# Optimization experiments

Measured on AMD Instinct MI355X. Metric: run time of the kernel, lower is better.

## Reference

```python
import jax, jax.numpy as jnp
import numpy as np

B, S, D = 1024, 60, 256   # seq_len=60 is hard-coded by nn.Linear(dim*60, n_experts)
H = 1024                  # d_inner
E = 8                     # n_experts
TOPK = 2
CAP = B * TOPK // E       # balanced per-expert capacity = 256


def setup_inputs() -> dict:
    key = jax.random.key(0)
    ks = jax.random.split(key, 9)
    s = 0.02
    return {
        "x":        jax.random.normal(ks[0], (B, S, D), dtype=jnp.float32),
        "W_switch": jax.random.normal(ks[1], (S * D, E), dtype=jnp.float32) * s,
        "b_switch": jnp.zeros((E,), dtype=jnp.float32),
        "W1":       jax.random.normal(ks[2], (E, D, H), dtype=jnp.float32) * s,
        "b1":       jnp.zeros((E, H), dtype=jnp.float32),
        "W2":       jax.random.normal(ks[3], (E, H, D), dtype=jnp.float32) * s,
        "b2":       jnp.zeros((E, D), dtype=jnp.float32),
        "gamma":    jnp.ones((D,), dtype=jnp.float32),
        "beta":     jnp.zeros((D,), dtype=jnp.float32),
    }


def reference(x, W_switch, b_switch, W1, b1, W2, b2, gamma, beta):
    # --- routing: softmax over experts per batch element ---
    logits = x.reshape(B, S * D) @ W_switch + b_switch          # [B, E]
    probs = jax.nn.softmax(logits, axis=-1)
    # balanced dispatch: each expert takes its top-CAP batch indices
    _, idx = jax.lax.top_k(probs.T, CAP)                        # [E, CAP] int32
    xe = x[idx]                                                 # gather -> [E, CAP, S, D]
    # --- per-expert grouped GEMMs (Column- then Row-parallel linear) ---
    h = jax.nn.gelu(jnp.einsum('ecsd,edh->ecsh', xe, W1)
                    + b1[:, None, None, :], approximate=False)  # [E, CAP, S, H]
    oe = jnp.einsum('ecsh,ehd->ecsd', h, W2) + b2[:, None, None, :]  # [E, CAP, S, D]
    # --- scatter-combine via index_add over the batch dim ---
    out = jnp.zeros_like(x).at[idx.reshape(-1)].add(oe.reshape(E * CAP, S, D))
    # --- residual + post-LayerNorm (pre_lnorm=False) ---
    z = x + out
    mu = jnp.mean(z, axis=-1, keepdims=True)
    var = jnp.var(z, axis=-1, keepdims=True)
    return (z - mu) * jax.lax.rsqrt(var + 1e-5) * gamma + beta
```

## Files before the change

### kernel.cpp

```cpp
#include <hip/hip_runtime.h>
#include <hip/hip_bf16.h>
#include <math.h>

#define NB   1024
#define NS   60
#define ND   256
#define NH   1024
#define NE   8
#define NCAP 256
#define NTOK (NCAP*NS)
#define BM   64
#define NBLK (NTOK/BM)

typedef __attribute__((ext_vector_type(8)))  short short8;
typedef __attribute__((ext_vector_type(16))) float floatx16;

__device__ __forceinline__ unsigned short f2bf(float f) {
    union { float f; unsigned u; } cv; cv.f = f;
    unsigned u = cv.u;
    u += 0x7FFFu + ((u >> 16) & 1u);
    return (unsigned short)(u >> 16);
}
__device__ __forceinline__ float bf2f(unsigned short h) {
    union { unsigned u; float f; } c; c.u = ((unsigned)h) << 16; return c.f;
}
__device__ __forceinline__ unsigned pk2bf(float a, float b) {
    return (unsigned)f2bf(a) | ((unsigned)f2bf(b) << 16);
}

__global__ void k_pack(const float* __restrict__ W1, const float* __restrict__ W2,
                       unsigned short* __restrict__ W1t, unsigned short* __restrict__ W2t) {
    int idx = blockIdx.x * 256 + threadIdx.x;
    if (idx < 524288) {
        int h4 = idx & 255;
        int k  = (idx >> 8) & 255;
        int e  = idx >> 16;
        float4 w = *(const float4*)(W1 + ((size_t)(e * 256 + k)) * 1024 + h4 * 4);
        float wv[4] = {w.x, w.y, w.z, w.w};
        int lane_k = ((k >> 3) & 1) * 32;
        int kt = k >> 4, j = k & 7;
#pragma unroll
        for (int c = 0; c < 4; ++c) {
            int h = h4 * 4 + c;
            int frag = (e * 32 + (h >> 5)) * 16 + kt;
            W1t[(size_t)frag * 512 + ((h & 31) + lane_k) * 8 + j] = f2bf(wv[c]);
        }
    } else {
        int i2 = idx - 524288;
        int d4 = i2 & 63;
        int h  = (i2 >> 6) & 1023;
        int e  = i2 >> 16;
        float4 w = *(const float4*)(W2 + ((size_t)(e * 1024 + h)) * 256 + d4 * 4);
        float wv[4] = {w.x, w.y, w.z, w.w};
        int lane_k = ((h >> 3) & 1) * 32;
        int kt = h >> 4, j = h & 7;
#pragma unroll
        for (int c = 0; c < 4; ++c) {
            int d = d4 * 4 + c;
            int frag = (e * 8 + (d >> 5)) * 64 + kt;
            W2t[(size_t)frag * 512 + ((d & 31) + lane_k) * 8 + j] = f2bf(wv[c]);
        }
    }
}

__global__ __launch_bounds__(256)
void k_route(const float* __restrict__ x, const float* __restrict__ Wsw,
             unsigned short* __restrict__ xb, float* __restrict__ partials) {
    int g = blockIdx.x & 127;
    int s = blockIdx.x >> 7;
    int team = threadIdx.x >> 5;
    int j = threadIdx.x & 31;
    int b = g * 8 + team;
    const float* xr = x + (size_t)b * 15360 + s * 1920;
    unsigned short* xbr = xb + (size_t)b * 15360 + s * 1920;
    float a[8];
#pragma unroll
    for (int e = 0; e < 8; ++e) a[e] = 0.f;
    for (int it = 0; it < 15; ++it) {
        int k = it * 128 + j * 4;
        float4 xv = *(const float4*)(xr + k);
        ushort4 o;
        o.x = f2bf(xv.x); o.y = f2bf(xv.y); o.z = f2bf(xv.z); o.w = f2bf(xv.w);
        *(ushort4*)(xbr + k) = o;
        float xa[4] = {xv.x, xv.y, xv.z, xv.w};
        const float* w = Wsw + (size_t)(s * 1920 + k) * 8;
#pragma unroll
        for (int c = 0; c < 4; ++c) {
            float4 w0 = *(const float4*)(w + c * 8);
            float4 w1 = *(const float4*)(w + c * 8 + 4);
            float xc = xa[c];
            a[0] += xc * w0.x; a[1] += xc * w0.y; a[2] += xc * w0.z; a[3] += xc * w0.w;
            a[4] += xc * w1.x; a[5] += xc * w1.y; a[6] += xc * w1.z; a[7] += xc * w1.w;
        }
    }
#pragma unroll
    for (int m = 16; m >= 1; m >>= 1) {
#pragma unroll
        for (int e = 0; e < 8; ++e) a[e] += __shfl_xor(a[e], m);
    }
    if (j == 0) {
        float4* p = (float4*)(partials + ((size_t)(s * 1024) + b) * 8);
        p[0] = make_float4(a[0], a[1], a[2], a[3]);
        p[1] = make_float4(a[4], a[5], a[6], a[7]);
    }
}

__global__ __launch_bounds__(256)
void k_topk(const float* __restrict__ partials, const float* __restrict__ bsw,
            int* __restrict__ idxb, int* __restrict__ cntb, int* __restrict__ slotb) {
    __shared__ float v[NB];
    int e = blockIdx.x >> 2;
    int q = blockIdx.x & 3;
    int tid = threadIdx.x;
    float bs[8];
#pragma unroll
    for (int i = 0; i < 8; ++i) bs[i] = bsw[i];
#pragma unroll
    for (int rr = 0; rr < 4; ++rr) {
        int row = rr * 256 + tid;
        float l[8];
#pragma unroll
        for (int i = 0; i < 8; ++i) l[i] = bs[i];
#pragma unroll
        for (int s = 0; s < 8; ++s) {
            const float4* p = (const float4*)(partials + ((size_t)(s * 1024) + row) * 8);
            float4 p0 = p[0], p1 = p[1];
            l[0] += p0.x; l[1] += p0.y; l[2] += p0.z; l[3] += p0.w;
            l[4] += p1.x; l[5] += p1.y; l[6] += p1.z; l[7] += p1.w;
        }
        float m = l[0];
#pragma unroll
        for (int i = 1; i < 8; ++i) m = fmaxf(m, l[i]);
        float sum = 0.f;
#pragma unroll
        for (int i = 0; i < 8; ++i) sum += expf(l[i] - m);
        v[row] = expf(l[e] - m) / sum;
    }
    __syncthreads();
    int cand = q * 256 + tid;
    float mv = v[cand];
    int cnt = 0;
    for (int jj = 0; jj < NB; ++jj) {
        float vj = v[jj];
        cnt += (vj > mv) || (vj == mv && jj < cand);
    }
    if (cnt < NCAP) {
        idxb[e * NCAP + cnt] = cand;
        int pos = atomicAdd(&cntb[cand], 1);
        slotb[cand * 8 + pos] = e * NCAP + cnt;
    }
}

__global__ __launch_bounds__(256, 2)
void k_mlp(const unsigned short* __restrict__ xb,
           const unsigned short* __restrict__ W1t,
           const unsigned short* __restrict__ W2t,
           const float* __restrict__ b1,
           const float* __restrict__ b2,
           const int* __restrict__ idxb,
           unsigned short* __restrict__ oe) {
    __shared__ __align__(16) unsigned short Alds[BM * 256];
    __shared__ __align__(16) unsigned short Plds[BM * 256];

    int e  = blockIdx.x / NBLK;
    int bm = blockIdx.x % NBLK;
    int tb = bm * BM;
    int tid = threadIdx.x;
    int lane = tid & 63, w = tid >> 6;
    int m31 = lane & 31, hi = lane >> 5;

    {
        int lr = tid >> 2;
        int s4 = tid & 3;
        int t = tb + lr;
        int c = t / 60;
        int s = t - c * 60;
        int bidx = idxb[e * NCAP + c];
        const unsigned short* src = xb + ((size_t)(bidx * 60 + s)) * 256;
#pragma unroll
        for (int jj = 0; jj < 8; ++jj) {
            int u = jj * 4 + s4;
            int up = u ^ (lr & 15);
            *(short8*)(&Alds[lr * 256 + up * 8]) = *(const short8*)(src + u * 8);
        }
    }
    __syncthreads();

    floatx16 acc2[2][2];
#pragma unroll
    for (int mt = 0; mt < 2; ++mt)
#pragma unroll
        for (int nt = 0; nt < 2; ++nt) acc2[mt][nt] = 0.f;

    for (int ch = 0; ch < 4; ++ch) {
        floatx16 pacc[2][2];
#pragma unroll
        for (int mt = 0; mt < 2; ++mt) { pacc[mt][0] = 0.f; pacc[mt][1] = 0.f; }
#pragma unroll 4
        for (int kt = 0; kt < 16; ++kt) {
            short8 bx[2];
#pragma unroll
            for (int nt = 0; nt < 2; ++nt) {
                int row = nt * 32 + m31;
                int up = (kt * 2 + hi) ^ (row & 15);
                bx[nt] = *(const short8*)(&Alds[row * 256 + up * 8]);
            }
#pragma unroll
            for (int mt = 0; mt < 2; ++mt) {
                int ht = ch * 8 + w * 2 + mt;
                short8 aw = *(const short8*)(W1t + ((size_t)((e * 32 + ht) * 16 + kt)) * 512 + lane * 8);
#pragma unroll
                for (int nt = 0; nt < 2; ++nt)
                    pacc[mt][nt] = __builtin_amdgcn_mfma_f32_32x32x16_bf16(aw, bx[nt], pacc[mt][nt], 0, 0, 0);
            }
        }
        __syncthreads();
#pragma unroll
        for (int mt = 0; mt < 2; ++mt) {
#pragma unroll
            for (int q = 0; q < 4; ++q) {
                int hh = w * 64 + mt * 32 + 8 * q + 4 * hi;
                float4 bb = *(const float4*)(b1 + e * NH + ch * 256 + hh);
                float bv[4] = {bb.x, bb.y, bb.z, bb.w};
#pragma unroll
                for (int nt = 0; nt < 2; ++nt) {
                    float g[4];
#pragma unroll
                    for (int r = 0; r < 4; ++r) {
                        float vv = pacc[mt][nt][4 * q + r] + bv[r];
                        float t2 = vv * vv;
                        float z = vv * fmaf(t2, -0.0713548162726f, -1.5957691216057308f);
                        g[r] = vv * __builtin_amdgcn_rcpf(1.0f + __expf(z));
                    }
                    int row = nt * 32 + m31;
                    int up = (hh >> 3) ^ (row & 15);
                    uint2 pk = {pk2bf(g[0], g[1]), pk2bf(g[2], g[3])};
                    *(uint2*)(&Plds[row * 256 + up * 8 + 4 * hi]) = pk;
                }
            }
        }
        __syncthreads();
#pragma unroll 4
        for (int kt = 0; kt < 16; ++kt) {
            short8 bp[2];
#pragma unroll
            for (int nt = 0; nt < 2; ++nt) {
                int row = nt * 32 + m31;
                int up = (kt * 2 + hi) ^ (row & 15);
                bp[nt] = *(const short8*)(&Plds[row * 256 + up * 8]);
            }
            int ktg = ch * 16 + kt;
#pragma unroll
            for (int mt = 0; mt < 2; ++mt) {
                int dt = w * 2 + mt;
                short8 aw = *(const short8*)(W2t + ((size_t)((e * 8 + dt) * 64 + ktg)) * 512 + lane * 8);
#pragma unroll
                for (int nt = 0; nt < 2; ++nt)
                    acc2[mt][nt] = __builtin_amdgcn_mfma_f32_32x32x16_bf16(aw, bp[nt], acc2[mt][nt], 0, 0, 0);
            }
        }
    }

    __syncthreads();
#pragma unroll
    for (int mt = 0; mt < 2; ++mt) {
#pragma unroll
        for (int q = 0; q < 4; ++q) {
            int dd = w * 64 + mt * 32 + 8 * q + 4 * hi;
            float4 bb = *(const float4*)(b2 + e * ND + dd);
            float bv[4] = {bb.x, bb.y, bb.z, bb.w};
#pragma unroll
            for (int nt = 0; nt < 2; ++nt) {
                int row = nt * 32 + m31;
                int up = (dd >> 3) ^ (row & 15);
                uint2 pk = {pk2bf(acc2[mt][nt][4 * q + 0] + bv[0], acc2[mt][nt][4 * q + 1] + bv[1]),
                            pk2bf(acc2[mt][nt][4 * q + 2] + bv[2], acc2[mt][nt][4 * q + 3] + bv[3])};
                *(uint2*)(&Plds[row * 256 + up * 8 + 4 * hi]) = pk;
            }
        }
    }
    __syncthreads();
    {
        int row = tid >> 2;
        int c = tid & 3;
        unsigned short* dst = oe + ((size_t)(e * NTOK + tb + row)) * 256;
#pragma unroll
        for (int uu = 0; uu < 8; ++uu) {
            int u = c + uu * 4;
            int up = u ^ (row & 15);
            *(short8*)(dst + u * 8) = *(const short8*)(&Plds[row * 256 + up * 8]);
        }
    }
}

__global__ void k_ln(const float* __restrict__ x, const unsigned short* __restrict__ oe,
                     const int* __restrict__ cntb, const int* __restrict__ slotb,
                     const float* __restrict__ gamma, const float* __restrict__ beta,
                     float* __restrict__ out) {
    int row = blockIdx.x * 4 + (threadIdx.x >> 6);
    int lane = threadIdx.x & 63;
    int b = row / 60;
    int s = row - b * 60;
    float4 v = ((const float4*)(x + (size_t)row * 256))[lane];
    int cnt = cntb[b];
    const int* sl = slotb + b * 8;
    for (int i = 0; i < cnt; ++i) {
        int slot = sl[i];
        ushort4 ov = ((const ushort4*)(oe + ((size_t)slot * 60 + s) * 256))[lane];
        v.x += bf2f(ov.x); v.y += bf2f(ov.y); v.z += bf2f(ov.z); v.w += bf2f(ov.w);
    }
    float sm = v.x + v.y + v.z + v.w;
    float q = v.x * v.x + v.y * v.y + v.z * v.z + v.w * v.w;
#pragma unroll
    for (int off = 32; off >= 1; off >>= 1) {
        sm += __shfl_xor(sm, off);
        q  += __shfl_xor(q, off);
    }
    float mu  = sm * (1.0f / 256.0f);
    float var = q * (1.0f / 256.0f) - mu * mu;
    float rs  = rsqrtf(var + 1e-5f);
    float4 g  = ((const float4*)gamma)[lane];
    float4 bt = ((const float4*)beta)[lane];
    float4 o;
    o.x = (v.x - mu) * rs * g.x + bt.x;
    o.y = (v.y - mu) * rs * g.y + bt.y;
    o.z = (v.z - mu) * rs * g.z + bt.z;
    o.w = (v.w - mu) * rs * g.w + bt.w;
    ((float4*)(out + (size_t)row * 256))[lane] = o;
}

extern "C" void kernel_launch(void* const* d_in, const int* in_sizes, int n_in,
                              void* d_out, int out_size, void* d_ws, size_t ws_size,
                              hipStream_t stream) {
    const float* x     = (const float*)d_in[0];
    const float* Wsw   = (const float*)d_in[1];
    const float* bsw   = (const float*)d_in[2];
    const float* W1    = (const float*)d_in[3];
    const float* b1    = (const float*)d_in[4];
    const float* W2    = (const float*)d_in[5];
    const float* b2    = (const float*)d_in[6];
    const float* gamma = (const float*)d_in[7];
    const float* beta  = (const float*)d_in[8];
    float* out = (float*)d_out;

    char* ws = (char*)d_ws;
    size_t off = 0;
    auto alloc = [&](size_t bytes) { void* p = ws + off; off += (bytes + 255) & ~255ull; return p; };
    float*          partials = (float*)alloc((size_t)8 * NB * NE * 4);
    int*            idxb     = (int*)alloc((size_t)NE * NCAP * 4);
    int*            cntb     = (int*)alloc((size_t)NB * 4);
    int*            slotb    = (int*)alloc((size_t)NB * 8 * 4);
    unsigned short* xb       = (unsigned short*)alloc((size_t)NB * NS * ND * 2);
    unsigned short* W1t      = (unsigned short*)alloc((size_t)NE * ND * NH * 2);
    unsigned short* W2t      = (unsigned short*)alloc((size_t)NE * NH * ND * 2);
    unsigned short* oe       = (unsigned short*)alloc((size_t)NE * NTOK * ND * 2);
    (void)ws_size; (void)in_sizes; (void)n_in; (void)out_size;

    hipMemsetAsync(cntb, 0, (size_t)NB * 4, stream);
    k_route<<<1024, 256, 0, stream>>>(x, Wsw, xb, partials);
    k_pack<<<4096, 256, 0, stream>>>(W1, W2, W1t, W2t);
    k_topk<<<32, 256, 0, stream>>>(partials, bsw, idxb, cntb, slotb);
    k_mlp<<<NE * NBLK, 256, 0, stream>>>(xb, W1t, W2t, b1, b2, idxb, oe);
    k_ln<<<NB * NS / 4, 256, 0, stream>>>(x, oe, cntb, slotb, gamma, beta, out);
}
```

Before: 442.8 us.

## Restructure MLP kernel LDS layout, add polynomial GELU, repack weights, fold memset

Stores X and the GELU output in LDS in MFMA-fragment order so each lane reads a contiguous short8 without swizzle math. It halves the P buffer by processing 128-wide hidden chunks over 8 iterations, and raises the occupancy hint to 3 blocks per CU. It also swaps the erf-style sigmoid GELU for a clamped polynomial, uses the hardware packed bf16 convert, and rewrites weight packing so each thread writes one 16-byte fragment. The cntb memset moves into the route kernel to drop a launch. The polynomial GELU changes numerics and the smaller chunks add more barriers.

```diff
diff --git a/kernel.cpp b/kernel.cpp
--- a/kernel.cpp
+++ b/kernel.cpp
@@ -24,48 +24,79 @@
 __device__ __forceinline__ float bf2f(unsigned short h) {
     union { unsigned u; float f; } c; c.u = ((unsigned)h) << 16; return c.f;
 }
-__device__ __forceinline__ unsigned pk2bf(float a, float b) {
+__device__ __forceinline__ unsigned cvt_pk_bf16(float a, float b) {
+#if defined(__has_builtin) && __has_builtin(__builtin_amdgcn_cvt_pk_bf16_f32)
+    typedef __attribute__((ext_vector_type(2))) __bf16 bf16x2;
+    union { bf16x2 v; unsigned u; } cc;
+    cc.v = __builtin_amdgcn_cvt_pk_bf16_f32(a, b);
+    return cc.u;
+#else
     return (unsigned)f2bf(a) | ((unsigned)f2bf(b) << 16);
-}
-
-__global__ void k_pack(const float* __restrict__ W1, const float* __restrict__ W2,
-                       unsigned short* __restrict__ W1t, unsigned short* __restrict__ W2t) {
+#endif
+}
+
+#define GELU_H0  0.39894228f
+#define GELU_H1 -0.065680755f
+#define GELU_H2  0.008727065f
+#define GELU_H3 -0.000664585f
+#define GELU_H4  2.07274e-5f
+__device__ __forceinline__ float fast_gelu(float xx) {
+    float t = __builtin_amdgcn_fmed3f(xx, -3.25f, 3.25f);
+    float s = t * t;
+    float p = fmaf(s, GELU_H4, GELU_H3);
+    p = fmaf(s, p, GELU_H2);
+    p = fmaf(s, p, GELU_H1);
+    p = fmaf(s, p, GELU_H0);
+    return xx * fmaf(t, p, 0.5f);
+}
+
+__global__ __launch_bounds__(256)
+void k_pack(const float* __restrict__ W1, const float* __restrict__ W2,
+            unsigned short* __restrict__ W1t, unsigned short* __restrict__ W2t) {
     int idx = blockIdx.x * 256 + threadIdx.x;
-    if (idx < 524288) {
-        int h4 = idx & 255;
-        int k  = (idx >> 8) & 255;
-        int e  = idx >> 16;
-        float4 w = *(const float4*)(W1 + ((size_t)(e * 256 + k)) * 1024 + h4 * 4);
-        float wv[4] = {w.x, w.y, w.z, w.w};
-        int lane_k = ((k >> 3) & 1) * 32;
-        int kt = k >> 4, j = k & 7;
-#pragma unroll
-        for (int c = 0; c < 4; ++c) {
-            int h = h4 * 4 + c;
-            int frag = (e * 32 + (h >> 5)) * 16 + kt;
-            W1t[(size_t)frag * 512 + ((h & 31) + lane_k) * 8 + j] = f2bf(wv[c]);
-        }
+    int lane = idx & 63;
+    int m31 = lane & 31, hi = lane >> 5;
+    const float* src;
+    unsigned short* dst;
+    int ldk;
+    if (idx < 262144) {
+        int fi = idx >> 6;
+        int kt = fi & 15;
+        int ht = (fi >> 4) & 31;
+        int e  = fi >> 9;
+        int k0 = kt * 16 + hi * 8;
+        int h  = ht * 32 + m31;
+        src = W1 + ((size_t)(e * 256 + k0)) * 1024 + h;
+        dst = W1t + (size_t)fi * 512 + lane * 8;
+        ldk = 1024;
     } else {
-        int i2 = idx - 524288;
-        int d4 = i2 & 63;
-        int h  = (i2 >> 6) & 1023;
-        int e  = i2 >> 16;
-        float4 w = *(const float4*)(W2 + ((size_t)(e * 1024 + h)) * 256 + d4 * 4);
-        float wv[4] = {w.x, w.y, w.z, w.w};
-        int lane_k = ((h >> 3) & 1) * 32;
-        int kt = h >> 4, j = h & 7;
-#pragma unroll
-        for (int c = 0; c < 4; ++c) {
-            int d = d4 * 4 + c;
-            int frag = (e * 8 + (d >> 5)) * 64 + kt;
-            W2t[(size_t)frag * 512 + ((d & 31) + lane_k) * 8 + j] = f2bf(wv[c]);
-        }
-    }
+        int i2 = idx - 262144;
+        int fi = i2 >> 6;
+        int kt = fi & 63;
+        int dt = (fi >> 6) & 7;
+        int e  = fi >> 9;
+        int k0 = kt * 16 + hi * 8;
+        int d  = dt * 32 + m31;
+        src = W2 + ((size_t)(e * 1024 + k0)) * 256 + d;
+        dst = W2t + (size_t)fi * 512 + lane * 8;
+        ldk = 256;
+    }
+    float v[8];
+#pragma unroll
+    for (int j = 0; j < 8; ++j) v[j] = src[(size_t)j * ldk];
+    uint4 o;
+    o.x = cvt_pk_bf16(v[0], v[1]);
+    o.y = cvt_pk_bf16(v[2], v[3]);
+    o.z = cvt_pk_bf16(v[4], v[5]);
+    o.w = cvt_pk_bf16(v[6], v[7]);
+    *(uint4*)dst = o;
 }
 
 __global__ __launch_bounds__(256)
 void k_route(const float* __restrict__ x, const float* __restrict__ Wsw,
-             unsigned short* __restrict__ xb, float* __restrict__ partials) {
+             unsigned short* __restrict__ xb, float* __restrict__ partials,
+             int* __restrict__ cntb) {
+    if (blockIdx.x < 4) cntb[blockIdx.x * 256 + threadIdx.x] = 0;
     int g = blockIdx.x & 127;
     int s = blockIdx.x >> 7;
     int team = threadIdx.x >> 5;
@@ -79,9 +110,8 @@
     for (int it = 0; it < 15; ++it) {
         int k = it * 128 + j * 4;
         float4 xv = *(const float4*)(xr + k);
-        ushort4 o;
-        o.x = f2bf(xv.x); o.y = f2bf(xv.y); o.z = f2bf(xv.z); o.w = f2bf(xv.w);
-        *(ushort4*)(xbr + k) = o;
+        uint2 pk = {cvt_pk_bf16(xv.x, xv.y), cvt_pk_bf16(xv.z, xv.w)};
+        *(uint2*)(xbr + k) = pk;
         float xa[4] = {xv.x, xv.y, xv.z, xv.w};
         const float* w = Wsw + (size_t)(s * 1920 + k) * 8;
 #pragma unroll
@@ -151,7 +181,7 @@
     }
 }
 
-__global__ __launch_bounds__(256, 2)
+__global__ __launch_bounds__(256, 3)
 void k_mlp(const unsigned short* __restrict__ xb,
            const unsigned short* __restrict__ W1t,
            const unsigned short* __restrict__ W2t,
@@ -159,8 +189,8 @@
            const float* __restrict__ b2,
            const int* __restrict__ idxb,
            unsigned short* __restrict__ oe) {
-    __shared__ __align__(16) unsigned short Alds[BM * 256];
-    __shared__ __align__(16) unsigned short Plds[BM * 256];
+    __shared__ __align__(16) unsigned short Xf[16384];
+    __shared__ __align__(16) unsigned short Pf[8192];
 
     int e  = blockIdx.x / NBLK;
     int bm = blockIdx.x % NBLK;
@@ -168,6 +198,8 @@
     int tid = threadIdx.x;
     int lane = tid & 63, w = tid >> 6;
     int m31 = lane & 31, hi = lane >> 5;
+    const short8* xfrag = (const short8*)Xf;
+    const short8* pfrag = (const short8*)Pf;
 
     {
         int lr = tid >> 2;
@@ -177,11 +209,13 @@
         int s = t - c * 60;
         int bidx = idxb[e * NCAP + c];
         const unsigned short* src = xb + ((size_t)(bidx * 60 + s)) * 256;
+        int nt = lr >> 5, mm = lr & 31;
 #pragma unroll
         for (int jj = 0; jj < 8; ++jj) {
             int u = jj * 4 + s4;
-            int up = u ^ (lr & 15);
-            *(short8*)(&Alds[lr * 256 + up * 8]) = *(const short8*)(src + u * 8);
+            int kt = u >> 1, uh = u & 1;
+            *(short8*)(&Xf[(((nt * 16 + kt) * 64) + uh * 32 + mm) * 8]) =
+                *(const short8*)(src + u * 8);
         }
     }
     __syncthreads();
@@ -192,76 +226,51 @@
 #pragma unroll
         for (int nt = 0; nt < 2; ++nt) acc2[mt][nt] = 0.f;
 
-    for (int ch = 0; ch < 4; ++ch) {
-        floatx16 pacc[2][2];
-#pragma unroll
-        for (int mt = 0; mt < 2; ++mt) { pacc[mt][0] = 0.f; pacc[mt][1] = 0.f; }
+    for (int ch = 0; ch < 8; ++ch) {
+        floatx16 pacc[2];
+        pacc[0] = 0.f; pacc[1] = 0.f;
+        int ht = ch * 4 + w;
+        const unsigned short* w1p = W1t + ((size_t)(e * 32 + ht) * 16) * 512 + lane * 8;
 #pragma unroll 4
         for (int kt = 0; kt < 16; ++kt) {
-            short8 bx[2];
+            short8 aw = *(const short8*)(w1p + (size_t)kt * 512);
+            short8 bx0 = xfrag[kt * 64 + lane];
+            short8 bx1 = xfrag[(16 + kt) * 64 + lane];
+            pacc[0] = __builtin_amdgcn_mfma_f32_32x32x16_bf16(aw, bx0, pacc[0], 0, 0, 0);
+            pacc[1] = __builtin_amdgcn_mfma_f32_32x32x16_bf16(aw, bx1, pacc[1], 0, 0, 0);
+        }
+        __syncthreads();
+        const float* b1c = b1 + e * NH + ch * 128 + w * 32;
+#pragma unroll
+        for (int q = 0; q < 4; ++q) {
+            float4 bb = *(const float4*)(b1c + 8 * q + 4 * hi);
+            float bv[4] = {bb.x, bb.y, bb.z, bb.w};
+            int ktp = w * 2 + (q >> 1);
 #pragma unroll
             for (int nt = 0; nt < 2; ++nt) {
-                int row = nt * 32 + m31;
-                int up = (kt * 2 + hi) ^ (row & 15);
-                bx[nt] = *(const short8*)(&Alds[row * 256 + up * 8]);
-            }
-#pragma unroll
-            for (int mt = 0; mt < 2; ++mt) {
-                int ht = ch * 8 + w * 2 + mt;
-                short8 aw = *(const short8*)(W1t + ((size_t)((e * 32 + ht) * 16 + kt)) * 512 + lane * 8);
-#pragma unroll
-                for (int nt = 0; nt < 2; ++nt)
-                    pacc[mt][nt] = __builtin_amdgcn_mfma_f32_32x32x16_bf16(aw, bx[nt], pacc[mt][nt], 0, 0, 0);
-            }
-        }
-        __syncthreads();
-#pragma unroll
-        for (int mt = 0; mt < 2; ++mt) {
-#pragma unroll
-            for (int q = 0; q < 4; ++q) {
-                int hh = w * 64 + mt * 32 + 8 * q + 4 * hi;
-                float4 bb = *(const float4*)(b1 + e * NH + ch * 256 + hh);
-                float bv[4] = {bb.x, bb.y, bb.z, bb.w};
-#pragma unroll
-                for (int nt = 0; nt < 2; ++nt) {
-                    float g[4];
-#pragma unroll
-                    for (int r = 0; r < 4; ++r) {
-                        float vv = pacc[mt][nt][4 * q + r] + bv[r];
-                        float t2 = vv * vv;
-                        float z = vv * fmaf(t2, -0.0713548162726f, -1.5957691216057308f);
-                        g[r] = vv * __builtin_amdgcn_rcpf(1.0f + __expf(z));
-                    }
-                    int row = nt * 32 + m31;
-                    int up = (hh >> 3) ^ (row & 15);
-                    uint2 pk = {pk2bf(g[0], g[1]), pk2bf(g[2], g[3])};
-                    *(uint2*)(&Plds[row * 256 + up * 8 + 4 * hi]) = pk;
-                }
+                float g[4];
+#pragma unroll
+                for (int r = 0; r < 4; ++r)
+                    g[r] = fast_gelu(pacc[nt][4 * q + r] + bv[r]);
+                uint2 pk = {cvt_pk_bf16(g[0], g[1]), cvt_pk_bf16(g[2], g[3])};
+                *(uint2*)(&Pf[(((nt * 8 + ktp) * 64) + (q & 1) * 32 + m31) * 8 + 4 * hi]) = pk;
             }
         }
         __syncthreads();
 #pragma unroll 4
-        for (int kt = 0; kt < 16; ++kt) {
-            short8 bp[2];
-#pragma unroll
-            for (int nt = 0; nt < 2; ++nt) {
-                int row = nt * 32 + m31;
-                int up = (kt * 2 + hi) ^ (row & 15);
-                bp[nt] = *(const short8*)(&Plds[row * 256 + up * 8]);
+        for (int kt = 0; kt < 8; ++kt) {
+            short8 bp0 = pfrag[kt * 64 + lane];
+            short8 bp1 = pfrag[(8 + kt) * 64 + lane];
+#pragma unroll
+            for (int mt = 0; mt < 2; ++mt) {
+                short8 aw = *(const short8*)(W2t +
+                    ((size_t)((e * 8 + w * 2 + mt) * 64 + ch * 8 + kt)) * 512 + lane * 8);
+                acc2[mt][0] = __builtin_amdgcn_mfma_f32_32x32x16_bf16(aw, bp0, acc2[mt][0], 0, 0, 0);
+                acc2[mt][1] = __builtin_amdgcn_mfma_f32_32x32x16_bf16(aw, bp1, acc2[mt][1], 0, 0, 0);
             }
-            int ktg = ch * 16 + kt;
-#pragma unroll
-            for (int mt = 0; mt < 2; ++mt) {
-                int dt = w * 2 + mt;
-                short8 aw = *(const short8*)(W2t + ((size_t)((e * 8 + dt) * 64 + ktg)) * 512 + lane * 8);
-#pragma unroll
-                for (int nt = 0; nt < 2; ++nt)
-                    acc2[mt][nt] = __builtin_amdgcn_mfma_f32_32x32x16_bf16(aw, bp[nt], acc2[mt][nt], 0, 0, 0);
-            }
-        }
-    }
-
-    __syncthreads();
+        }
+    }
+
 #pragma unroll
     for (int mt = 0; mt < 2; ++mt) {
 #pragma unroll
@@ -269,13 +278,16 @@
             int dd = w * 64 + mt * 32 + 8 * q + 4 * hi;
             float4 bb = *(const float4*)(b2 + e * ND + dd);
             float bv[4] = {bb.x, bb.y, bb.z, bb.w};
+            int u16 = dd >> 3;
 #pragma unroll
             for (int nt = 0; nt < 2; ++nt) {
                 int row = nt * 32 + m31;
-                int up = (dd >> 3) ^ (row & 15);
-                uint2 pk = {pk2bf(acc2[mt][nt][4 * q + 0] + bv[0], acc2[mt][nt][4 * q + 1] + bv[1]),
-                            pk2bf(acc2[mt][nt][4 * q + 2] + bv[2], acc2[mt][nt][4 * q + 3] + bv[3])};
-                *(uint2*)(&Plds[row * 256 + up * 8 + 4 * hi]) = pk;
+                int up = u16 ^ (row & 15);
+                uint2 pk = {cvt_pk_bf16(acc2[mt][nt][4 * q + 0] + bv[0],
+                                        acc2[mt][nt][4 * q + 1] + bv[1]),
+                            cvt_pk_bf16(acc2[mt][nt][4 * q + 2] + bv[2],
+                                        acc2[mt][nt][4 * q + 3] + bv[3])};
+                *(uint2*)(&Xf[row * 256 + up * 8 + 4 * hi]) = pk;
             }
         }
     }
@@ -288,7 +300,7 @@
         for (int uu = 0; uu < 8; ++uu) {
             int u = c + uu * 4;
             int up = u ^ (row & 15);
-            *(short8*)(dst + u * 8) = *(const short8*)(&Plds[row * 256 + up * 8]);
+            *(short8*)(dst + u * 8) = *(const short8*)(&Xf[row * 256 + up * 8]);
         }
     }
 }
@@ -356,9 +368,8 @@
     unsigned short* oe       = (unsigned short*)alloc((size_t)NE * NTOK * ND * 2);
     (void)ws_size; (void)in_sizes; (void)n_in; (void)out_size;
 
-    hipMemsetAsync(cntb, 0, (size_t)NB * 4, stream);
-    k_route<<<1024, 256, 0, stream>>>(x, Wsw, xb, partials);
-    k_pack<<<4096, 256, 0, stream>>>(W1, W2, W1t, W2t);
+    k_route<<<1024, 256, 0, stream>>>(x, Wsw, xb, partials, cntb);
+    k_pack<<<2048, 256, 0, stream>>>(W1, W2, W1t, W2t);
     k_topk<<<32, 256, 0, stream>>>(partials, bsw, idxb, cntb, slotb);
     k_mlp<<<NE * NBLK, 256, 0, stream>>>(xb, W1t, W2t, b1, b2, idxb, oe);
     k_ln<<<NB * NS / 4, 256, 0, stream>>>(x, oe, cntb, slotb, gamma, beta, out);
```

Result: faster. 395.1 us (-10.8%).
